# Kernel tuning notes

Measured on AMD Instinct MI355X. Metric: run time of the kernel, lower is better.

Reference implementation:

```python
import jax, jax.numpy as jnp
import numpy as np
from jax.ops import segment_sum

NEG_SLOPE = 0.2
N0, N1, N2, N3 = 100000, 300000, 150000, 50000
DIN, DMID = 64, 128


def setup_inputs() -> dict:
    key = jax.random.key(0)
    ks = jax.random.split(key, 16)
    g = lambda k, shp, fan_in: jax.random.normal(k, shp, dtype=jnp.float32) * (1.0 / np.sqrt(fan_in))
    return {
        "x_0": jax.random.normal(ks[0], (N0, DIN), dtype=jnp.float32),
        "x_1": jax.random.normal(ks[1], (N1, DIN), dtype=jnp.float32),
        "x_2": jax.random.normal(ks[2], (N2, DIN), dtype=jnp.float32),
        "x_3": jax.random.normal(ks[3], (N3, DIN), dtype=jnp.float32),
        "x_4": jax.random.normal(ks[4], (10000, DIN), dtype=jnp.float32),
        # COO indices: row 0 = destination (row of sparse matrix), row 1 = source (column)
        "adj0_idx": jax.random.randint(ks[5], (2, 800000), 0, N0),
        "adj3_idx": jax.random.randint(ks[6], (2, 800000), 0, N3),
        "inc01_t": jax.random.randint(ks[7], (600000,), 0, N0),   # rows of incidence_0_1 (0-cells)
        "inc01_s": jax.random.randint(ks[8], (600000,), 0, N1),   # cols (1-cells)
        "inc23_t": jax.random.randint(ks[9], (200000,), 0, N2),   # rows of incidence_2_3 (2-cells)
        "inc23_s": jax.random.randint(ks[10], (200000,), 0, N3),  # cols (3-cells)
        "W_hbs0": g(ks[11], (DIN, DMID), DIN),
        "W_hbs3": g(ks[12], (DIN, DMID), DIN),
        "W_s01": g(ks[13], (DIN, DMID), DIN),   # HBNS source weight: x_1 -> target-rank (0) messages
        "W_t23": g(ks[14], (DIN, DMID), DIN),   # HBNS target weight: x_2 -> source-rank (3) messages
        "fc0_W": g(ks[15], (DMID, DMID), DMID),
        "fc0_b": jnp.zeros((DMID,), dtype=jnp.float32),
        "fc3_W": g(jax.random.fold_in(key, 100), (DMID, DMID), DMID),
        "fc3_b": jnp.zeros((DMID,), dtype=jnp.float32),
    }


def _spmm(msg, dst, src, n_out):
    # out[i] = sum_{(i,j) in nnz} msg[j]  == sparse_matrix @ msg
    return segment_sum(msg[src], dst, num_segments=n_out)


def reference(x_0, x_1, x_2, x_3, x_4, adj0_idx, adj3_idx, inc01_t, inc01_s,
              inc23_t, inc23_s, W_hbs0, W_hbs3, W_s01, W_t23,
              fc0_W, fc0_b, fc3_W, fc3_b):
    lrelu = lambda v: jax.nn.leaky_relu(v, NEG_SLOPE)
    # HBS within-rank propagation: A @ (x W)
    x_0_to_0 = _spmm(x_0 @ W_hbs0, adj0_idx[0], adj0_idx[1], x_0.shape[0])
    x_3_to_3 = _spmm(x_3 @ W_hbs3, adj3_idx[0], adj3_idx[1], x_3.shape[0])
    # HBNS cross-rank propagation
    # message on target rank 0: incidence_0_1 @ (x_1 W_s)
    x_1_to_0 = _spmm(x_1 @ W_s01, inc01_t, inc01_s, x_0.shape[0])
    # message on source rank 3: incidence_2_3^T @ (x_2 W_t)
    x_2_to_3 = _spmm(x_2 @ W_t23, inc23_s, inc23_t, x_3.shape[0])
    # sum aggregation + FC + LeakyReLU
    x_0_new = lrelu((x_0_to_0 + x_1_to_0) @ fc0_W.T + fc0_b)
    x_3_new = lrelu((x_2_to_3 + x_3_to_3) @ fc3_W.T + fc3_b)
    return (x_0_new, x_1, x_2, x_3_new, x_4)
```

## Files before the change

### kernel.cpp

```cpp
#include <hip/hip_runtime.h>

#define NEG_SLOPE 0.2f


__global__ __launch_bounds__(256) void hist_all(const int* __restrict__ ad0,
                                                const int* __restrict__ d1,
                                                const int* __restrict__ ad3,
                                                const int* __restrict__ d2,
                                                int E0, int E01, int E3, int E23,
                                                int n0, int n3,
                                                int* __restrict__ counts) {
    int T = E0 + E01 + E3 + E23;
    int i = blockIdx.x * 256 + threadIdx.x;
    int stride = gridDim.x * 256;
    for (; i < T; i += stride) {
        int j = i, d, base;
        if (j < E0) { d = ad0[j]; base = 0; }
        else if ((j -= E0) < E01) { d = d1[j]; base = n0; }
        else if ((j -= E01) < E3) { d = ad3[j]; base = 2 * n0; }
        else { j -= E3; d = d2[j]; base = 2 * n0 + n3; }
        atomicAdd(&counts[base + d], 1);
    }
}

__global__ __launch_bounds__(256) void chunk_sum(const int* __restrict__ counts,
                                                 int* __restrict__ bsum, int NT) {
    __shared__ int red[256];
    int base = blockIdx.x * 2048;
    int t = threadIdx.x;
    int s = 0;
#pragma unroll
    for (int j = 0; j < 8; ++j) {
        int idx = base + j * 256 + t;
        if (idx < NT) s += counts[idx];
    }
    red[t] = s;
    __syncthreads();
    for (int off = 128; off > 0; off >>= 1) {
        if (t < off) red[t] += red[t + off];
        __syncthreads();
    }
    if (t == 0) bsum[blockIdx.x] = red[0];
}

__global__ __launch_bounds__(256) void scan_bsum(const int* __restrict__ bsum,
                                                 int* __restrict__ bbase, int nb) {
    __shared__ int sh[256];
    int t = threadIdx.x;
    int v = (t < nb) ? bsum[t] : 0;
    sh[t] = v;
    __syncthreads();
    for (int off = 1; off < 256; off <<= 1) {
        int add = (t >= off) ? sh[t - off] : 0;
        __syncthreads();
        sh[t] += add;
        __syncthreads();
    }
    if (t < nb) bbase[t] = sh[t] - v;
}

__global__ __launch_bounds__(256) void chunk_scan(const int* __restrict__ counts,
                                                  const int* __restrict__ bbase,
                                                  int* __restrict__ offsets,
                                                  int* __restrict__ cursors,
                                                  int NT, int E_total) {
    __shared__ int tsum[256];
    int t = threadIdx.x;
    int base = blockIdx.x * 2048 + t * 8;
    int v[8];
    int s = 0;
#pragma unroll
    for (int j = 0; j < 8; ++j) {
        int idx = base + j;
        v[j] = (idx < NT) ? counts[idx] : 0;
        s += v[j];
    }
    tsum[t] = s;
    __syncthreads();
    for (int off = 1; off < 256; off <<= 1) {
        int add = (t >= off) ? tsum[t - off] : 0;
        __syncthreads();
        tsum[t] += add;
        __syncthreads();
    }
    int run = bbase[blockIdx.x] + tsum[t] - s;
#pragma unroll
    for (int j = 0; j < 8; ++j) {
        int idx = base + j;
        if (idx < NT) { offsets[idx] = run; cursors[idx] = run; }
        run += v[j];
    }
    if (blockIdx.x == 0 && t == 0) offsets[NT] = E_total;
}

__global__ __launch_bounds__(256) void fill_all(const int* __restrict__ ad0,
                                                const int* __restrict__ as0,
                                                const int* __restrict__ d1,
                                                const int* __restrict__ s1,
                                                const int* __restrict__ ad3,
                                                const int* __restrict__ as3,
                                                const int* __restrict__ d2,
                                                const int* __restrict__ s2,
                                                int E0, int E01, int E3, int E23,
                                                int n0, int n3,
                                                int* __restrict__ cursors,
                                                int* __restrict__ edge_src) {
    int T = E0 + E01 + E3 + E23;
    int i = blockIdx.x * 256 + threadIdx.x;
    int stride = gridDim.x * 256;
    for (; i < T; i += stride) {
        int j = i, d, s, base;
        if (j < E0) { d = ad0[j]; s = as0[j]; base = 0; }
        else if ((j -= E0) < E01) { d = d1[j]; s = s1[j]; base = n0; }
        else if ((j -= E01) < E3) { d = ad3[j]; s = as3[j]; base = 2 * n0; }
        else { j -= E3; d = d2[j]; s = s2[j]; base = 2 * n0 + n3; }
        int pos = atomicAdd(&cursors[base + d], 1);
        edge_src[pos] = s;
    }
}

__global__ __launch_bounds__(256) void gather_kernel(const int* __restrict__ offsets,
                                                     const int* __restrict__ edge_src,
                                                     const float* __restrict__ x0,
                                                     const float* __restrict__ x1,
                                                     const float* __restrict__ x2,
                                                     const float* __restrict__ x3,
                                                     float* __restrict__ agg0,
                                                     float* __restrict__ agg3,
                                                     int n0, int n3) {
    const int NT = 2 * n0 + 2 * n3;
    int row = blockIdx.x * 4 + (threadIdx.x >> 6);
    if (row >= NT) return;
    int lane = threadIdx.x & 63;
    int g = lane >> 4;
    int c4 = (lane & 15) * 4;
    const float* xs;
    float* outp;
    if (row < n0)               { xs = x0; outp = &agg0[(size_t)row * 128]; }
    else if (row < 2 * n0)      { xs = x1; outp = &agg0[(size_t)(row - n0) * 128 + 64]; }
    else if (row < 2 * n0 + n3) { xs = x3; outp = &agg3[(size_t)(row - 2 * n0) * 128]; }
    else                        { xs = x2; outp = &agg3[(size_t)(row - 2 * n0 - n3) * 128 + 64]; }

    int beg = offsets[row], end = offsets[row + 1];
    float4 acc = make_float4(0.f, 0.f, 0.f, 0.f);
    int k = beg;
    for (; k + 8 <= end; k += 8) {
        int i0 = edge_src[k + g];
        int i1 = edge_src[k + 4 + g];
        float4 a = *(const float4*)&xs[(size_t)i0 * 64 + c4];
        float4 b = *(const float4*)&xs[(size_t)i1 * 64 + c4];
        acc.x += a.x; acc.y += a.y; acc.z += a.z; acc.w += a.w;
        acc.x += b.x; acc.y += b.y; acc.z += b.z; acc.w += b.w;
    }
    int rem = end - k;
    if (g < rem) {
        int i0 = edge_src[k + g];
        float4 a = *(const float4*)&xs[(size_t)i0 * 64 + c4];
        acc.x += a.x; acc.y += a.y; acc.z += a.z; acc.w += a.w;
    }
    if (rem > 4 && g < rem - 4) {
        int i1 = edge_src[k + 4 + g];
        float4 b = *(const float4*)&xs[(size_t)i1 * 64 + c4];
        acc.x += b.x; acc.y += b.y; acc.z += b.z; acc.w += b.w;
    }
#pragma unroll
    for (int d = 16; d < 64; d <<= 1) {
        acc.x += __shfl_xor(acc.x, d, 64);
        acc.y += __shfl_xor(acc.y, d, 64);
        acc.z += __shfl_xor(acc.z, d, 64);
        acc.w += __shfl_xor(acc.w, d, 64);
    }
    if (g == 0) *(float4*)&outp[c4] = acc;
}

__global__ __launch_bounds__(256) void combine_w2(const float* __restrict__ Wtop0,
                                                  const float* __restrict__ Wbot0,
                                                  const float* __restrict__ F0,
                                                  float* __restrict__ WC0,
                                                  const float* __restrict__ Wtop3,
                                                  const float* __restrict__ Wbot3,
                                                  const float* __restrict__ F3,
                                                  float* __restrict__ WC3) {
    int gi = blockIdx.x * 256 + threadIdx.x;
    int which = gi >> 14;
    int i = gi & 16383;
    const float* Wtop = which ? Wtop3 : Wtop0;
    const float* Wbot = which ? Wbot3 : Wbot0;
    const float* F = which ? F3 : F0;
    float* WC = which ? WC3 : WC0;
    int k = i >> 7;
    int c = i & 127;
    const float* wrow = (k < 64) ? &Wtop[(size_t)k * 128] : &Wbot[(size_t)(k - 64) * 128];
    const float* frow = &F[(size_t)c * 128];
    float s = 0.f;
#pragma unroll 8
    for (int j = 0; j < 128; j += 4) {
        float4 w = *(const float4*)&wrow[j];
        float4 f = *(const float4*)&frow[j];
        s = fmaf(w.x, f.x, s);
        s = fmaf(w.y, f.y, s);
        s = fmaf(w.z, f.z, s);
        s = fmaf(w.w, f.w, s);
    }
    WC[(size_t)k * 128 + c] = s;
}

__global__ __launch_bounds__(256) void fc_lrelu(const float* __restrict__ A,
                                                const float* __restrict__ WC,
                                                const float* __restrict__ bias,
                                                float* __restrict__ Y, int n) {
    __shared__ float WS[64][128];
    __shared__ float XS[64][68];
    const int t = threadIdx.x;
    const int row0 = blockIdx.x * 64;
    const int c = (t & 31) * 4;
    const int rbase = (t >> 5) * 8;
    float acc[8][4];
#pragma unroll
    for (int i = 0; i < 8; ++i)
#pragma unroll
        for (int j = 0; j < 4; ++j) acc[i][j] = 0.f;

    for (int p = 0; p < 2; ++p) {
        __syncthreads();
        const float4* Wp4 = (const float4*)(WC + (size_t)p * 64 * 128);
        float4* WS4 = (float4*)&WS[0][0];
        for (int i = t; i < 2048; i += 256) WS4[i] = Wp4[i];
        for (int i = t; i < 64 * 16; i += 256) {
            int r = i >> 4, c4 = i & 15;
            float4 v = make_float4(0.f, 0.f, 0.f, 0.f);
            if (row0 + r < n)
                v = *(const float4*)&A[(size_t)(row0 + r) * 128 + p * 64 + c4 * 4];
            *(float4*)&XS[r][c4 * 4] = v;
        }
        __syncthreads();

#pragma unroll 4
        for (int k = 0; k < 64; k += 4) {
            float4 w[4];
            w[0] = *(const float4*)&WS[k + 0][c];
            w[1] = *(const float4*)&WS[k + 1][c];
            w[2] = *(const float4*)&WS[k + 2][c];
            w[3] = *(const float4*)&WS[k + 3][c];
#pragma unroll
            for (int i = 0; i < 8; ++i) {
                float4 x = *(const float4*)&XS[rbase + i][k];
                float xs[4] = {x.x, x.y, x.z, x.w};
#pragma unroll
                for (int kk = 0; kk < 4; ++kk) {
                    acc[i][0] = fmaf(xs[kk], w[kk].x, acc[i][0]);
                    acc[i][1] = fmaf(xs[kk], w[kk].y, acc[i][1]);
                    acc[i][2] = fmaf(xs[kk], w[kk].z, acc[i][2]);
                    acc[i][3] = fmaf(xs[kk], w[kk].w, acc[i][3]);
                }
            }
        }
    }

    float4 b = *(const float4*)&bias[c];
    float bs[4] = {b.x, b.y, b.z, b.w};
#pragma unroll
    for (int i = 0; i < 8; ++i) {
        int r = row0 + rbase + i;
        if (r < n) {
            float o[4];
#pragma unroll
            for (int j = 0; j < 4; ++j) {
                float v = acc[i][j] + bs[j];
                o[j] = v > 0.f ? v : NEG_SLOPE * v;
            }
            *(float4*)&Y[(size_t)r * 128 + c] = make_float4(o[0], o[1], o[2], o[3]);
        }
    }
}

__global__ __launch_bounds__(256) void copy_all(const float4* __restrict__ s1, float4* __restrict__ o1, int m1,
                                                const float4* __restrict__ s2, float4* __restrict__ o2, int m2,
                                                const float4* __restrict__ s4, float4* __restrict__ o4, int m4) {
    int total = m1 + m2 + m4;
    int i = blockIdx.x * 256 + threadIdx.x;
    int stride = gridDim.x * 256;
    for (; i < total; i += stride) {
        int j = i;
        if (j < m1) { o1[j] = s1[j]; }
        else if ((j -= m1) < m2) { o2[j] = s2[j]; }
        else { j -= m2; o4[j] = s4[j]; }
    }
}

extern "C" void kernel_launch(void* const* d_in, const int* in_sizes, int n_in,
                              void* d_out, int out_size, void* d_ws, size_t ws_size,
                              hipStream_t stream) {
    const float* x0 = (const float*)d_in[0];
    const float* x1 = (const float*)d_in[1];
    const float* x2 = (const float*)d_in[2];
    const float* x3 = (const float*)d_in[3];
    const float* x4 = (const float*)d_in[4];
    const int* adj0 = (const int*)d_in[5];
    const int* adj3 = (const int*)d_in[6];
    const int* inc01_t = (const int*)d_in[7];
    const int* inc01_s = (const int*)d_in[8];
    const int* inc23_t = (const int*)d_in[9];
    const int* inc23_s = (const int*)d_in[10];
    const float* W_hbs0 = (const float*)d_in[11];
    const float* W_hbs3 = (const float*)d_in[12];
    const float* W_s01 = (const float*)d_in[13];
    const float* W_t23 = (const float*)d_in[14];
    const float* fc0_W = (const float*)d_in[15];
    const float* fc0_b = (const float*)d_in[16];
    const float* fc3_W = (const float*)d_in[17];
    const float* fc3_b = (const float*)d_in[18];

    const int n0 = in_sizes[0] / 64, n1 = in_sizes[1] / 64;
    const int n2 = in_sizes[2] / 64, n3 = in_sizes[3] / 64, n4 = in_sizes[4] / 64;
    const int E0 = in_sizes[5] / 2, E3 = in_sizes[6] / 2;
    const int E01 = in_sizes[7], E23 = in_sizes[9];
    const int NT = 2 * n0 + 2 * n3;
    const int E_total = E0 + E01 + E3 + E23;
    const int nb = (NT + 2047) / 2048;

    float* ws = (float*)d_ws;
    size_t off = 0;
    float* agg0 = ws + off; off += (size_t)n0 * 128;
    float* agg3 = ws + off; off += (size_t)n3 * 128;
    float* wc0 = ws + off;  off += 16384;
    float* wc3 = ws + off;  off += 16384;
    int* counts = (int*)(ws + off);   off += NT;
    int* offsets = (int*)(ws + off);  off += NT + 1;
    int* cursors = (int*)(ws + off);  off += NT;
    int* bsum = (int*)(ws + off);     off += 256;
    int* bbase = (int*)(ws + off);    off += 256;
    int* edge_src = (int*)(ws + off); off += E_total;

    float* out = (float*)d_out;
    float* o_x0 = out;
    float* o_x1 = o_x0 + (size_t)n0 * 128;
    float* o_x2 = o_x1 + (size_t)n1 * 64;
    float* o_x3 = o_x2 + (size_t)n2 * 64;
    float* o_x4 = o_x3 + (size_t)n3 * 128;

    hipMemsetAsync(counts, 0, (size_t)NT * sizeof(int), stream);
    hist_all<<<(E_total + 255) / 256, 256, 0, stream>>>(
        adj0, inc01_t, adj3, inc23_s, E0, E01, E3, E23, n0, n3, counts);
    chunk_sum<<<nb, 256, 0, stream>>>(counts, bsum, NT);
    scan_bsum<<<1, 256, 0, stream>>>(bsum, bbase, nb);
    chunk_scan<<<nb, 256, 0, stream>>>(counts, bbase, offsets, cursors, NT, E_total);
    fill_all<<<(E_total + 255) / 256, 256, 0, stream>>>(
        adj0, adj0 + E0, inc01_t, inc01_s, adj3, adj3 + E3, inc23_s, inc23_t,
        E0, E01, E3, E23, n0, n3, cursors, edge_src);

    gather_kernel<<<(NT + 3) / 4, 256, 0, stream>>>(offsets, edge_src, x0, x1, x2, x3,
                                                    agg0, agg3, n0, n3);

    combine_w2<<<128, 256, 0, stream>>>(W_hbs0, W_s01, fc0_W, wc0,
                                        W_hbs3, W_t23, fc3_W, wc3);
    fc_lrelu<<<(n0 + 63) / 64, 256, 0, stream>>>(agg0, wc0, fc0_b, o_x0, n0);
    fc_lrelu<<<(n3 + 63) / 64, 256, 0, stream>>>(agg3, wc3, fc3_b, o_x3, n3);

    copy_all<<<8192, 256, 0, stream>>>((const float4*)x1, (float4*)o_x1, n1 * 16,
                                       (const float4*)x2, (float4*)o_x2, n2 * 16,
                                       (const float4*)x4, (float4*)o_x4, n4 * 16);
}
```

Before: 800.7 us.

## Pad histogram counters to separate cache lines and batch atomics in CSR build

Counters for the per-destination histogram and fill cursors are padded to a stride of 16 ints (64 bytes) so each atomic hits its own line, and the cursor array is merged into the padded count array. hist_all and fill_all move to a fixed 2048-block grid with a 4-way unrolled loop, so several independent atomics are in flight per thread, and edge_src is written with nontemporal stores. The aim is less contention on the atomics and more memory-level parallelism. The cost is a 16x larger memset (about 10 MB) and strided, poorly coalesced reads in chunk_sum and chunk_scan.

```diff
diff --git a/kernel.cpp b/kernel.cpp
--- a/kernel.cpp
+++ b/kernel.cpp
@@ -1,6 +1,7 @@
 #include <hip/hip_runtime.h>
 
 #define NEG_SLOPE 0.2f
+#define CPAD 16
 
 
 __global__ __launch_bounds__(256) void hist_all(const int* __restrict__ ad0,
@@ -9,21 +10,26 @@
                                                 const int* __restrict__ d2,
                                                 int E0, int E01, int E3, int E23,
                                                 int n0, int n3,
-                                                int* __restrict__ counts) {
+                                                int* __restrict__ counts_p) {
     int T = E0 + E01 + E3 + E23;
-    int i = blockIdx.x * 256 + threadIdx.x;
     int stride = gridDim.x * 256;
-    for (; i < T; i += stride) {
-        int j = i, d, base;
-        if (j < E0) { d = ad0[j]; base = 0; }
-        else if ((j -= E0) < E01) { d = d1[j]; base = n0; }
-        else if ((j -= E01) < E3) { d = ad3[j]; base = 2 * n0; }
-        else { j -= E3; d = d2[j]; base = 2 * n0 + n3; }
-        atomicAdd(&counts[base + d], 1);
-    }
-}
-
-__global__ __launch_bounds__(256) void chunk_sum(const int* __restrict__ counts,
+    for (int i = blockIdx.x * 256 + threadIdx.x; i < T; i += 4 * stride) {
+#pragma unroll
+        for (int u = 0; u < 4; ++u) {
+            int idx = i + u * stride;
+            if (idx < T) {
+                int j = idx, d, base;
+                if (j < E0) { d = ad0[j]; base = 0; }
+                else if ((j -= E0) < E01) { d = d1[j]; base = n0; }
+                else if ((j -= E01) < E3) { d = ad3[j]; base = 2 * n0; }
+                else { j -= E3; d = d2[j]; base = 2 * n0 + n3; }
+                atomicAdd(&counts_p[(base + d) * CPAD], 1);
+            }
+        }
+    }
+}
+
+__global__ __launch_bounds__(256) void chunk_sum(const int* __restrict__ counts_p,
                                                  int* __restrict__ bsum, int NT) {
     __shared__ int red[256];
     int base = blockIdx.x * 2048;
@@ -32,7 +38,7 @@
 #pragma unroll
     for (int j = 0; j < 8; ++j) {
         int idx = base + j * 256 + t;
-        if (idx < NT) s += counts[idx];
+        if (idx < NT) s += counts_p[idx * CPAD];
     }
     red[t] = s;
     __syncthreads();
@@ -59,10 +65,9 @@
     if (t < nb) bbase[t] = sh[t] - v;
 }
 
-__global__ __launch_bounds__(256) void chunk_scan(const int* __restrict__ counts,
+__global__ __launch_bounds__(256) void chunk_scan(int* __restrict__ counts_p,
                                                   const int* __restrict__ bbase,
                                                   int* __restrict__ offsets,
-                                                  int* __restrict__ cursors,
                                                   int NT, int E_total) {
     __shared__ int tsum[256];
     int t = threadIdx.x;
@@ -72,7 +77,7 @@
 #pragma unroll
     for (int j = 0; j < 8; ++j) {
         int idx = base + j;
-        v[j] = (idx < NT) ? counts[idx] : 0;
+        v[j] = (idx < NT) ? counts_p[idx * CPAD] : 0;
         s += v[j];
     }
     tsum[t] = s;
@@ -87,7 +92,7 @@
 #pragma unroll
     for (int j = 0; j < 8; ++j) {
         int idx = base + j;
-        if (idx < NT) { offsets[idx] = run; cursors[idx] = run; }
+        if (idx < NT) { offsets[idx] = run; counts_p[idx * CPAD] = run; }
         run += v[j];
     }
     if (blockIdx.x == 0 && t == 0) offsets[NT] = E_total;
@@ -103,19 +108,34 @@
                                                 const int* __restrict__ s2,
                                                 int E0, int E01, int E3, int E23,
                                                 int n0, int n3,
-                                                int* __restrict__ cursors,
+                                                int* __restrict__ cursors_p,
                                                 int* __restrict__ edge_src) {
     int T = E0 + E01 + E3 + E23;
-    int i = blockIdx.x * 256 + threadIdx.x;
     int stride = gridDim.x * 256;
-    for (; i < T; i += stride) {
-        int j = i, d, s, base;
-        if (j < E0) { d = ad0[j]; s = as0[j]; base = 0; }
-        else if ((j -= E0) < E01) { d = d1[j]; s = s1[j]; base = n0; }
-        else if ((j -= E01) < E3) { d = ad3[j]; s = as3[j]; base = 2 * n0; }
-        else { j -= E3; d = d2[j]; s = s2[j]; base = 2 * n0 + n3; }
-        int pos = atomicAdd(&cursors[base + d], 1);
-        edge_src[pos] = s;
+    for (int i = blockIdx.x * 256 + threadIdx.x; i < T; i += 4 * stride) {
+        int dv[4], sv[4];
+        bool ok[4];
+#pragma unroll
+        for (int u = 0; u < 4; ++u) {
+            int idx = i + u * stride;
+            ok[u] = idx < T;
+            if (ok[u]) {
+                int j = idx, d, s, base;
+                if (j < E0) { d = ad0[j]; s = as0[j]; base = 0; }
+                else if ((j -= E0) < E01) { d = d1[j]; s = s1[j]; base = n0; }
+                else if ((j -= E01) < E3) { d = ad3[j]; s = as3[j]; base = 2 * n0; }
+                else { j -= E3; d = d2[j]; s = s2[j]; base = 2 * n0 + n3; }
+                dv[u] = base + d;
+                sv[u] = s;
+            }
+        }
+        int pos[4];
+#pragma unroll
+        for (int u = 0; u < 4; ++u)
+            if (ok[u]) pos[u] = atomicAdd(&cursors_p[dv[u] * CPAD], 1);
+#pragma unroll
+        for (int u = 0; u < 4; ++u)
+            if (ok[u]) __builtin_nontemporal_store(sv[u], &edge_src[pos[u]]);
     }
 }
 
@@ -325,9 +345,8 @@
     float* agg3 = ws + off; off += (size_t)n3 * 128;
     float* wc0 = ws + off;  off += 16384;
     float* wc3 = ws + off;  off += 16384;
-    int* counts = (int*)(ws + off);   off += NT;
+    int* counts_p = (int*)(ws + off); off += (size_t)NT * CPAD;
     int* offsets = (int*)(ws + off);  off += NT + 1;
-    int* cursors = (int*)(ws + off);  off += NT;
     int* bsum = (int*)(ws + off);     off += 256;
     int* bbase = (int*)(ws + off);    off += 256;
     int* edge_src = (int*)(ws + off); off += E_total;
@@ -339,15 +358,15 @@
     float* o_x3 = o_x2 + (size_t)n2 * 64;
     float* o_x4 = o_x3 + (size_t)n3 * 128;
 
-    hipMemsetAsync(counts, 0, (size_t)NT * sizeof(int), stream);
-    hist_all<<<(E_total + 255) / 256, 256, 0, stream>>>(
-        adj0, inc01_t, adj3, inc23_s, E0, E01, E3, E23, n0, n3, counts);
-    chunk_sum<<<nb, 256, 0, stream>>>(counts, bsum, NT);
+    hipMemsetAsync(counts_p, 0, (size_t)NT * CPAD * sizeof(int), stream);
+    hist_all<<<2048, 256, 0, stream>>>(
+        adj0, inc01_t, adj3, inc23_s, E0, E01, E3, E23, n0, n3, counts_p);
+    chunk_sum<<<nb, 256, 0, stream>>>(counts_p, bsum, NT);
     scan_bsum<<<1, 256, 0, stream>>>(bsum, bbase, nb);
-    chunk_scan<<<nb, 256, 0, stream>>>(counts, bbase, offsets, cursors, NT, E_total);
-    fill_all<<<(E_total + 255) / 256, 256, 0, stream>>>(
+    chunk_scan<<<nb, 256, 0, stream>>>(counts_p, bbase, offsets, NT, E_total);
+    fill_all<<<2048, 256, 0, stream>>>(
         adj0, adj0 + E0, inc01_t, inc01_s, adj3, adj3 + E3, inc23_s, inc23_t,
-        E0, E01, E3, E23, n0, n3, cursors, edge_src);
+        E0, E01, E3, E23, n0, n3, counts_p, edge_src);
 
     gather_kernel<<<(NT + 3) / 4, 256, 0, stream>>>(offsets, edge_src, x0, x1, x2, x3,
                                                     agg0, agg3, n0, n3);
```

Measured after the change: 860.7 us. 7.5% more time.

## Partition CSR fill by destination range and use 16-lane rows in gather

Applied to the files above, without the earlier changes.

The CSR fill kernel now splits destination rows into 16 partitions. Each group of blocks scans all edges but only scatters those whose destination falls in its range, so atomics and edge_src writes stay localized in cache. The cost is rereading the destination indices 16 times. The gather kernel now gives each row 16 lanes instead of 64, with sequential 2-way unrolled accumulation and no cross-lane shuffle reduction, so 16 rows run per block.

```diff
diff --git a/kernel.cpp b/kernel.cpp
--- a/kernel.cpp
+++ b/kernel.cpp
@@ -1,6 +1,7 @@
 #include <hip/hip_runtime.h>
 
 #define NEG_SLOPE 0.2f
+#define NPART 16
 
 
 __global__ __launch_bounds__(256) void hist_all(const int* __restrict__ ad0,
@@ -93,47 +94,57 @@
     if (blockIdx.x == 0 && t == 0) offsets[NT] = E_total;
 }
 
-__global__ __launch_bounds__(256) void fill_all(const int* __restrict__ ad0,
-                                                const int* __restrict__ as0,
-                                                const int* __restrict__ d1,
-                                                const int* __restrict__ s1,
-                                                const int* __restrict__ ad3,
-                                                const int* __restrict__ as3,
-                                                const int* __restrict__ d2,
-                                                const int* __restrict__ s2,
-                                                int E0, int E01, int E3, int E23,
-                                                int n0, int n3,
-                                                int* __restrict__ cursors,
-                                                int* __restrict__ edge_src) {
+__global__ __launch_bounds__(256) void fill_part(const int* __restrict__ ad0,
+                                                 const int* __restrict__ as0,
+                                                 const int* __restrict__ d1,
+                                                 const int* __restrict__ s1,
+                                                 const int* __restrict__ ad3,
+                                                 const int* __restrict__ as3,
+                                                 const int* __restrict__ d2,
+                                                 const int* __restrict__ s2,
+                                                 int E0, int E01, int E3, int E23,
+                                                 int n0, int n3, int PS,
+                                                 int* __restrict__ cursors,
+                                                 int* __restrict__ edge_src) {
     int T = E0 + E01 + E3 + E23;
-    int i = blockIdx.x * 256 + threadIdx.x;
-    int stride = gridDim.x * 256;
-    for (; i < T; i += stride) {
-        int j = i, d, s, base;
-        if (j < E0) { d = ad0[j]; s = as0[j]; base = 0; }
-        else if ((j -= E0) < E01) { d = d1[j]; s = s1[j]; base = n0; }
-        else if ((j -= E01) < E3) { d = ad3[j]; s = as3[j]; base = 2 * n0; }
-        else { j -= E3; d = d2[j]; s = s2[j]; base = 2 * n0 + n3; }
-        int pos = atomicAdd(&cursors[base + d], 1);
-        edge_src[pos] = s;
-    }
-}
-
-__global__ __launch_bounds__(256) void gather_kernel(const int* __restrict__ offsets,
-                                                     const int* __restrict__ edge_src,
-                                                     const float* __restrict__ x0,
-                                                     const float* __restrict__ x1,
-                                                     const float* __restrict__ x2,
-                                                     const float* __restrict__ x3,
-                                                     float* __restrict__ agg0,
-                                                     float* __restrict__ agg3,
-                                                     int n0, int n3) {
+    int p = blockIdx.x & (NPART - 1);
+    int bp = blockIdx.x / NPART;
+    int nbp = gridDim.x / NPART;
+    int lo = p * PS, hi = lo + PS;
+    int stride = nbp * 256;
+    for (int i = bp * 256 + threadIdx.x; i < T; i += stride) {
+        int j = i, d, base;
+        if (j < E0) { d = ad0[j]; base = 0; }
+        else if ((j -= E0) < E01) { d = d1[j]; base = n0; }
+        else if ((j -= E01) < E3) { d = ad3[j]; base = 2 * n0; }
+        else { j -= E3; d = d2[j]; base = 2 * n0 + n3; }
+        int cd = base + d;
+        if (cd >= lo && cd < hi) {
+            int s;
+            int jj = i;
+            if (jj < E0) s = as0[jj];
+            else if ((jj -= E0) < E01) s = s1[jj];
+            else if ((jj -= E01) < E3) s = as3[jj];
+            else { jj -= E3; s = s2[jj]; }
+            int pos = atomicAdd(&cursors[cd], 1);
+            edge_src[pos] = s;
+        }
+    }
+}
+
+__global__ __launch_bounds__(256) void gather4(const int* __restrict__ offsets,
+                                               const int* __restrict__ edge_src,
+                                               const float* __restrict__ x0,
+                                               const float* __restrict__ x1,
+                                               const float* __restrict__ x2,
+                                               const float* __restrict__ x3,
+                                               float* __restrict__ agg0,
+                                               float* __restrict__ agg3,
+                                               int n0, int n3) {
     const int NT = 2 * n0 + 2 * n3;
-    int row = blockIdx.x * 4 + (threadIdx.x >> 6);
+    int row = blockIdx.x * 16 + (threadIdx.x >> 4);
+    int c4 = (threadIdx.x & 15) * 4;
     if (row >= NT) return;
-    int lane = threadIdx.x & 63;
-    int g = lane >> 4;
-    int c4 = (lane & 15) * 4;
     const float* xs;
     float* outp;
     if (row < n0)               { xs = x0; outp = &agg0[(size_t)row * 128]; }
@@ -141,36 +152,24 @@
     else if (row < 2 * n0 + n3) { xs = x3; outp = &agg3[(size_t)(row - 2 * n0) * 128]; }
     else                        { xs = x2; outp = &agg3[(size_t)(row - 2 * n0 - n3) * 128 + 64]; }
 
-    int beg = offsets[row], end = offsets[row + 1];
+    int k = offsets[row], end = offsets[row + 1];
     float4 acc = make_float4(0.f, 0.f, 0.f, 0.f);
-    int k = beg;
-    for (; k + 8 <= end; k += 8) {
-        int i0 = edge_src[k + g];
-        int i1 = edge_src[k + 4 + g];
+    for (; k + 2 <= end; k += 2) {
+        int i0 = edge_src[k];
+        int i1 = edge_src[k + 1];
         float4 a = *(const float4*)&xs[(size_t)i0 * 64 + c4];
         float4 b = *(const float4*)&xs[(size_t)i1 * 64 + c4];
-        acc.x += a.x; acc.y += a.y; acc.z += a.z; acc.w += a.w;
-        acc.x += b.x; acc.y += b.y; acc.z += b.z; acc.w += b.w;
-    }
-    int rem = end - k;
-    if (g < rem) {
-        int i0 = edge_src[k + g];
+        acc.x += a.x + b.x;
+        acc.y += a.y + b.y;
+        acc.z += a.z + b.z;
+        acc.w += a.w + b.w;
+    }
+    if (k < end) {
+        int i0 = edge_src[k];
         float4 a = *(const float4*)&xs[(size_t)i0 * 64 + c4];
         acc.x += a.x; acc.y += a.y; acc.z += a.z; acc.w += a.w;
     }
-    if (rem > 4 && g < rem - 4) {
-        int i1 = edge_src[k + 4 + g];
-        float4 b = *(const float4*)&xs[(size_t)i1 * 64 + c4];
-        acc.x += b.x; acc.y += b.y; acc.z += b.z; acc.w += b.w;
-    }
-#pragma unroll
-    for (int d = 16; d < 64; d <<= 1) {
-        acc.x += __shfl_xor(acc.x, d, 64);
-        acc.y += __shfl_xor(acc.y, d, 64);
-        acc.z += __shfl_xor(acc.z, d, 64);
-        acc.w += __shfl_xor(acc.w, d, 64);
-    }
-    if (g == 0) *(float4*)&outp[c4] = acc;
+    *(float4*)&outp[c4] = acc;
 }
 
 __global__ __launch_bounds__(256) void combine_w2(const float* __restrict__ Wtop0,
@@ -318,6 +317,7 @@
     const int NT = 2 * n0 + 2 * n3;
     const int E_total = E0 + E01 + E3 + E23;
     const int nb = (NT + 2047) / 2048;
+    const int PS = (NT + NPART - 1) / NPART;
 
     float* ws = (float*)d_ws;
     size_t off = 0;
@@ -345,12 +345,12 @@
     chunk_sum<<<nb, 256, 0, stream>>>(counts, bsum, NT);
     scan_bsum<<<1, 256, 0, stream>>>(bsum, bbase, nb);
     chunk_scan<<<nb, 256, 0, stream>>>(counts, bbase, offsets, cursors, NT, E_total);
-    fill_all<<<(E_total + 255) / 256, 256, 0, stream>>>(
+    fill_part<<<NPART * 256, 256, 0, stream>>>(
         adj0, adj0 + E0, inc01_t, inc01_s, adj3, adj3 + E3, inc23_s, inc23_t,
-        E0, E01, E3, E23, n0, n3, cursors, edge_src);
-
-    gather_kernel<<<(NT + 3) / 4, 256, 0, stream>>>(offsets, edge_src, x0, x1, x2, x3,
-                                                    agg0, agg3, n0, n3);
+        E0, E01, E3, E23, n0, n3, PS, cursors, edge_src);
+
+    gather4<<<(NT + 15) / 16, 256, 0, stream>>>(offsets, edge_src, x0, x1, x2, x3,
+                                                agg0, agg3, n0, n3);
 
     combine_w2<<<128, 256, 0, stream>>>(W_hbs0, W_s01, fc0_W, wc0,
                                         W_hbs3, W_t23, fc3_W, wc3);
```

After: 726.3 us. 9.3% less time.
